# Performance work log

Hardware: AMD Instinct MI355X
Metric: run time of the kernel (lower is better)

Reference implementation:

```python
import jax, jax.numpy as jnp
import numpy as np

LN_EPS = 1e-5
H_STEP = 0.1


def _mm(W, x):
    # conv1d with kernel size 1 == channel matmul: [O,C] x [B,C,N] -> [B,O,N]
    return jnp.einsum('oc,bcn->bon', W, x)


def _layer_norm_all(x):
    # F.layer_norm(x, x.shape): normalize over the ENTIRE tensor, no affine
    m = jnp.mean(x)
    v = jnp.mean((x - m) ** 2)
    return (x - m) * jax.lax.rsqrt(v + LN_EPS)


def double_layer(x, K1, K2):
    # dropout omitted (eval mode / deterministic reference)
    x = _mm(K1, x)
    x = _layer_norm_all(x)
    x = jax.nn.relu(x)
    return _mm(K2, x)


def setup_inputs() -> dict:
    key = jax.random.key(0)
    ks = jax.random.split(key, 16)
    B, XIN, EIN, HID, OUT, NL = 1, 32, 32, 128, 64, 4
    N, E = 50000, 500000
    stdv = 0.001
    inp = {
        'xn': jax.random.normal(ks[0], (B, XIN, N), dtype=jnp.float32),
        'xe': jax.random.normal(ks[1], (B, EIN, E), dtype=jnp.float32),
        'iInd': jax.random.randint(ks[2], (E,), 0, N),
        'jInd': jax.random.randint(ks[3], (E,), 0, N),
        'K1Nopen': jax.random.normal(ks[4], (HID, XIN), dtype=jnp.float32) * stdv,
        'K2Nopen': jax.random.normal(ks[5], (HID, HID), dtype=jnp.float32) * stdv,
        'K1Eopen': jax.random.normal(ks[6], (HID, EIN), dtype=jnp.float32) * stdv,
        'K2Eopen': jax.random.normal(ks[7], (HID, HID), dtype=jnp.float32) * stdv,
        'KNout': jax.random.normal(ks[8], (OUT, HID), dtype=jnp.float32) * stdv,
        'KE1': jax.random.normal(ks[9], (NL, 2 * HID, 3 * HID), dtype=jnp.float32) * stdv,
        'KE2': jax.random.normal(ks[10], (NL, HID, 2 * HID), dtype=jnp.float32) * stdv,
        'KN1': jax.random.normal(ks[11], (NL, 2 * HID, 3 * HID), dtype=jnp.float32) * stdv,
        'KN2': jax.random.normal(ks[12], (NL, HID, 2 * HID), dtype=jnp.float32) * stdv,
    }
    return inp


def reference(xn, xe, iInd, jInd, K1Nopen, K2Nopen, K1Eopen, K2Eopen, KNout,
              KE1, KE2, KN1, KN2):
    xn = double_layer(xn, K1Nopen, K2Nopen)
    xe = double_layer(xe, K1Eopen, K2Eopen)
    N = xn.shape[2]
    # Source sets row = col = Graph.iInd (faithful replication)
    row = iInd
    col = iInd
    nlayers = KE1.shape[0]
    for i in range(nlayers):
        # gather node feats to edges, concat with edge feats: [B, 3*hid, E]
        xec = jnp.concatenate([xn[:, :, row], xn[:, :, col], xe], axis=1)
        xec = double_layer(xec, KE1[i], KE2[i])
        # scatter edge feats back to both endpoints
        zeros = jnp.zeros((xec.shape[0], xec.shape[1], N), dtype=xec.dtype)
        s_i = zeros.at[:, :, iInd].add(xec)
        s_j = zeros.at[:, :, jInd].add(xec)
        ave = 0.5 * (s_i + s_j)          # edgeAve(method='ave')
        div = s_i - s_j                   # edgeDiv
        xnc = jnp.concatenate([ave, div, xn], axis=1)
        xnc = double_layer(xnc, KN1[i], KN2[i])
        xn = xn + H_STEP * xnc
        xe = xe + H_STEP * xec
    xn = _mm(KNout, xn)
    return xn, xe
```

## Files before the change

kernel.cpp:

```cpp
#include <hip/hip_runtime.h>
#include <hip/hip_bf16.h>


typedef __hip_bfloat16 bf16;
typedef __attribute__((ext_vector_type(8))) short bf16x8;
typedef __attribute__((ext_vector_type(4))) float f32x4;

#define HSTEP 0.1f

__device__ __forceinline__ bf16  f2b(float v){ return __float2bfloat16(v); }
__device__ __forceinline__ unsigned int f2bu(float v){
    return (unsigned int)__builtin_bit_cast(unsigned short, __float2bfloat16(v));
}
__device__ __forceinline__ void store8(float* p, const float* a){
    *(float4*)p       = make_float4(a[0],a[1],a[2],a[3]);
    *((float4*)p + 1) = make_float4(a[4],a[5],a[6],a[7]);
}

__device__ __forceinline__ uint4 lnrelu_pack(uint4 r, float mean, float rstd){
    float f0 = __uint_as_float(r.x << 16), f1 = __uint_as_float(r.x & 0xffff0000u);
    float f2 = __uint_as_float(r.y << 16), f3 = __uint_as_float(r.y & 0xffff0000u);
    float f4 = __uint_as_float(r.z << 16), f5 = __uint_as_float(r.z & 0xffff0000u);
    float f6 = __uint_as_float(r.w << 16), f7 = __uint_as_float(r.w & 0xffff0000u);
    f0 = fmaxf(0.f,(f0-mean)*rstd); f1 = fmaxf(0.f,(f1-mean)*rstd);
    f2 = fmaxf(0.f,(f2-mean)*rstd); f3 = fmaxf(0.f,(f3-mean)*rstd);
    f4 = fmaxf(0.f,(f4-mean)*rstd); f5 = fmaxf(0.f,(f5-mean)*rstd);
    f6 = fmaxf(0.f,(f6-mean)*rstd); f7 = fmaxf(0.f,(f7-mean)*rstd);
    uint4 q;
    q.x = f2bu(f0) | (f2bu(f1) << 16);
    q.y = f2bu(f2) | (f2bu(f3) << 16);
    q.z = f2bu(f4) | (f2bu(f5) << 16);
    q.w = f2bu(f6) | (f2bu(f7) << 16);
    return q;
}
__device__ __forceinline__ uint4 pack8f(float4 a, float4 b){
    uint4 q;
    q.x = f2bu(a.x) | (f2bu(a.y) << 16);
    q.y = f2bu(a.z) | (f2bu(a.w) << 16);
    q.z = f2bu(b.x) | (f2bu(b.y) << 16);
    q.w = f2bu(b.z) | (f2bu(b.w) << 16);
    return q;
}

__global__ void wt_transpose(const float* __restrict__ src, float* __restrict__ dst,
                             int O, int C) {
    int i = blockIdx.x*256 + threadIdx.x;
    if (i >= O*C) return;
    int o = i / C, c = i - o*C;
    dst[c*O + o] = src[i];
}

__global__ void wt_ke1_bf(const float* __restrict__ src, bf16* __restrict__ dst) {
    int i = blockIdx.x*256 + threadIdx.x;
    if (i >= 256*256) return;
    int o = i >> 8, c = i & 255;
    float v;
    if (c < 128) v = src[o*384 + c] + src[o*384 + 128 + c];
    else         v = src[o*384 + 128 + c];
    dst[i] = f2b(v);
}

__global__ void wt_cast_bf(const float* __restrict__ src, bf16* __restrict__ dst, int cnt) {
    int i = blockIdx.x*256 + threadIdx.x;
    if (i < cnt) dst[i] = f2b(src[i]);
}

__global__ void csr_hist(const int* __restrict__ ind, int* __restrict__ cnt, int E){
    int e = blockIdx.x*256 + threadIdx.x;
    if (e < E) atomicAdd(&cnt[ind[e]], 1);
}

__global__ void csr_scan(const int* __restrict__ cnt, int* __restrict__ rowptr,
                         int* __restrict__ cursor, int Nn)
{
    __shared__ int part[256];
    int tx = threadIdx.x;
    int chunk = (Nn + 255) / 256;
    int a0 = tx * chunk;
    int a1 = a0 + chunk; if (a1 > Nn) a1 = Nn; if (a0 > Nn) a0 = Nn;
    int s = 0;
    for (int i = a0; i < a1; ++i) s += cnt[i];
    part[tx] = s;
    __syncthreads();
    for (int d = 1; d < 256; d <<= 1) {
        int v = (tx >= d) ? part[tx - d] : 0;
        __syncthreads();
        part[tx] += v;
        __syncthreads();
    }
    int run = (tx == 0) ? 0 : part[tx - 1];
    for (int i = a0; i < a1; ++i) {
        rowptr[i] = run; cursor[i] = run;
        run += cnt[i];
    }
    if (tx == 255) rowptr[Nn] = run;
}

__global__ void csr_fill(const int* __restrict__ ind, int* __restrict__ cursor,
                         int* __restrict__ eadj, int E){
    int e = blockIdx.x*256 + threadIdx.x;
    if (e < E) {
        int p = atomicAdd(&cursor[ind[e]], 1);
        eadj[p] = e;
    }
}

template<bool YB16>
__launch_bounds__(256)
__global__ void gather_nodes(const void* __restrict__ yv,
                             const int* __restrict__ rowptr,
                             const int* __restrict__ eadj,
                             float* __restrict__ s, int Nn)
{
    int wid  = threadIdx.x >> 6;
    int lane = threadIdx.x & 63;
    int node = blockIdx.x * 4 + wid;
    if (node >= Nn) return;
    int k0 = rowptr[node], k1 = rowptr[node+1];
    float a0 = 0.f, a1 = 0.f;
    for (int k = k0; k < k1; ++k) {
        int e = eadj[k];
        if constexpr (YB16) {
            unsigned int b = *((const unsigned int*)yv + (size_t)e*64 + lane);
            a0 += __uint_as_float(b << 16);
            a1 += __uint_as_float(b & 0xffff0000u);
        } else {
            float2 v = *((const float2*)yv + (size_t)e*64 + lane);
            a0 += v.x; a1 += v.y;
        }
    }
    *(float2*)(s + (size_t)node*128 + lane*2) = make_float2(a0, a1);
}

__global__ void ln_reduce(const double* __restrict__ redp, int nb,
                          float* __restrict__ ln, double cnt)
{
    __shared__ double s0[256], s1[256];
    int tx = threadIdx.x;
    double a = 0.0, b = 0.0;
    for (int i = tx; i < nb; i += 256) { a += redp[2*i]; b += redp[2*i+1]; }
    s0[tx] = a; s1[tx] = b;
    __syncthreads();
    for (int s = 128; s > 0; s >>= 1) {
        if (tx < s) { s0[tx] += s0[tx+s]; s1[tx] += s1[tx+s]; }
        __syncthreads();
    }
    if (tx == 0) {
        double m = s0[0] / cnt;
        double var = s1[0] / cnt - m*m;
        if (var < 0.0) var = 0.0;
        ln[0] = (float)m;
        ln[1] = (float)(1.0 / sqrt(var + 1e-5));
    }
}

__launch_bounds__(256)
__global__ void mfma_mm1_edge(const bf16* __restrict__ Wb,
                              const bf16* __restrict__ xnb,
                              const float* __restrict__ xe,
                              const int* __restrict__ iInd,
                              bf16* __restrict__ ucm,
                              int E, double* __restrict__ redp)
{
    __shared__ __align__(16) unsigned short Vs[64*256];
    __shared__ double sred[512];
    const int tx = threadIdx.x;
    const int x0 = blockIdx.x * 64;
    const int e = tx >> 2, q4 = tx & 3;
    const int xedge = x0 + e;
    const bool ev = xedge < E;
    const int gidx = ev ? iInd[xedge] : 0;
    const unsigned swz = (unsigned)((e & 7) << 3);

    #pragma unroll
    for (int p = 0; p < 4; ++p) {
        int k0 = q4*8 + p*32;
        uint4 v = make_uint4(0,0,0,0);
        if (ev) v = *(const uint4*)(xnb + (size_t)gidx*128 + k0);
        *(uint4*)&Vs[(unsigned)(e*256 + k0) ^ swz] = v;
    }
    #pragma unroll
    for (int p = 0; p < 4; ++p) {
        int k0 = q4*8 + p*32;
        uint4 v = make_uint4(0,0,0,0);
        if (ev) {
            const float* s = xe + (size_t)xedge*128 + k0;
            v = pack8f(*(const float4*)s, *(const float4*)(s + 4));
        }
        *(uint4*)&Vs[(unsigned)(e*256 + 128 + k0) ^ swz] = v;
    }
    __syncthreads();

    const int w = tx >> 6, l = tx & 63;
    const int colb = l & 15, grp = l >> 4;
    f32x4 acc[4][4];
    #pragma unroll
    for (int m=0;m<4;++m)
        #pragma unroll
        for (int n=0;n<4;++n) acc[m][n] = (f32x4){0.f,0.f,0.f,0.f};

    #pragma unroll
    for (int kc = 0; kc < 8; ++kc) {
        const int kf = kc*32 + grp*8;
        bf16x8 a[4], b[4];
        #pragma unroll
        for (int m=0;m<4;++m) {
            int row = w*64 + m*16 + colb;
            a[m] = __builtin_bit_cast(bf16x8, *(const uint4*)(Wb + row*256 + kf));
        }
        #pragma unroll
        for (int n=0;n<4;++n) {
            int ee = n*16 + colb;
            b[n] = __builtin_bit_cast(bf16x8,
                     *(const uint4*)&Vs[(unsigned)(ee*256 + kf) ^ (unsigned)((ee&7)<<3)]);
        }
        #pragma unroll
        for (int m=0;m<4;++m)
            #pragma unroll
            for (int n=0;n<4;++n)
                acc[m][n] = __builtin_amdgcn_mfma_f32_16x16x32_bf16(a[m], b[n], acc[m][n], 0, 0, 0);
    }

    double ls = 0.0, ls2 = 0.0;
    const int rq = grp*4;
    #pragma unroll
    for (int n=0;n<4;++n) {
        int edge = x0 + n*16 + colb;
        if (edge < E) {
            #pragma unroll
            for (int m=0;m<4;++m) {
                f32x4 v = acc[m][n];
                int r0 = w*64 + m*16 + rq;
                uint2 q;
                q.x = f2bu(v[0]) | (f2bu(v[1]) << 16);
                q.y = f2bu(v[2]) | (f2bu(v[3]) << 16);
                *(uint2*)(ucm + (size_t)edge*256 + r0) = q;
                ls  += (double)v[0] + (double)v[1] + (double)v[2] + (double)v[3];
                ls2 += (double)v[0]*v[0] + (double)v[1]*v[1]
                     + (double)v[2]*v[2] + (double)v[3]*v[3];
            }
        }
    }
    sred[tx] = ls; sred[256+tx] = ls2;
    __syncthreads();
    for (int s=128; s>0; s>>=1) {
        if (tx < s) { sred[tx] += sred[tx+s]; sred[256+tx] += sred[256+tx+s]; }
        __syncthreads();
    }
    if (tx == 0) {
        redp[2*(size_t)blockIdx.x]     = sred[0];
        redp[2*(size_t)blockIdx.x + 1] = sred[256];
    }
}

__launch_bounds__(256)
__global__ void mfma_mm1_node(const bf16* __restrict__ Wb,
                              const float* __restrict__ si,
                              const float* __restrict__ sj,
                              const float* __restrict__ xn,
                              bf16* __restrict__ ucm,
                              int Nn, double* __restrict__ redp)
{
    __shared__ __align__(16) unsigned short Vs[64*384];
    __shared__ double sred[512];
    const int tx = threadIdx.x;
    const int x0 = blockIdx.x * 64;
    const int e = tx >> 2, q4 = tx & 3;
    const int node = x0 + e;
    const bool nv = node < Nn;
    const unsigned swz = (unsigned)((e & 7) << 3);

    #pragma unroll
    for (int p = 0; p < 4; ++p) {
        int k0 = q4*8 + p*32;
        uint4 va = make_uint4(0,0,0,0), vd = va;
        if (nv) {
            const float* ps = si + (size_t)node*128 + k0;
            const float* pt = sj + (size_t)node*128 + k0;
            float4 a0 = *(const float4*)ps, a1 = *(const float4*)(ps+4);
            float4 b0 = *(const float4*)pt, b1 = *(const float4*)(pt+4);
            float4 av0 = make_float4(0.5f*(a0.x+b0.x),0.5f*(a0.y+b0.y),
                                     0.5f*(a0.z+b0.z),0.5f*(a0.w+b0.w));
            float4 av1 = make_float4(0.5f*(a1.x+b1.x),0.5f*(a1.y+b1.y),
                                     0.5f*(a1.z+b1.z),0.5f*(a1.w+b1.w));
            float4 dv0 = make_float4(a0.x-b0.x,a0.y-b0.y,a0.z-b0.z,a0.w-b0.w);
            float4 dv1 = make_float4(a1.x-b1.x,a1.y-b1.y,a1.z-b1.z,a1.w-b1.w);
            va = pack8f(av0, av1);
            vd = pack8f(dv0, dv1);
        }
        *(uint4*)&Vs[(unsigned)(e*384 + k0) ^ swz] = va;
        *(uint4*)&Vs[(unsigned)(e*384 + 128 + k0) ^ swz] = vd;
    }
    #pragma unroll
    for (int p = 0; p < 4; ++p) {
        int k0 = q4*8 + p*32;
        uint4 v = make_uint4(0,0,0,0);
        if (nv) {
            const float* s = xn + (size_t)node*128 + k0;
            v = pack8f(*(const float4*)s, *(const float4*)(s + 4));
        }
        *(uint4*)&Vs[(unsigned)(e*384 + 256 + k0) ^ swz] = v;
    }
    __syncthreads();

    const int w = tx >> 6, l = tx & 63;
    const int colb = l & 15, grp = l >> 4;
    f32x4 acc[4][4];
    #pragma unroll
    for (int m=0;m<4;++m)
        #pragma unroll
        for (int n=0;n<4;++n) acc[m][n] = (f32x4){0.f,0.f,0.f,0.f};

    #pragma unroll
    for (int kc = 0; kc < 12; ++kc) {
        const int kf = kc*32 + grp*8;
        bf16x8 a[4], b[4];
        #pragma unroll
        for (int m=0;m<4;++m) {
            int row = w*64 + m*16 + colb;
            a[m] = __builtin_bit_cast(bf16x8, *(const uint4*)(Wb + row*384 + kf));
        }
        #pragma unroll
        for (int n=0;n<4;++n) {
            int ee = n*16 + colb;
            b[n] = __builtin_bit_cast(bf16x8,
                     *(const uint4*)&Vs[(unsigned)(ee*384 + kf) ^ (unsigned)((ee&7)<<3)]);
        }
        #pragma unroll
        for (int m=0;m<4;++m)
            #pragma unroll
            for (int n=0;n<4;++n)
                acc[m][n] = __builtin_amdgcn_mfma_f32_16x16x32_bf16(a[m], b[n], acc[m][n], 0, 0, 0);
    }

    double ls = 0.0, ls2 = 0.0;
    const int rq = grp*4;
    #pragma unroll
    for (int n=0;n<4;++n) {
        int nd = x0 + n*16 + colb;
        if (nd < Nn) {
            #pragma unroll
            for (int m=0;m<4;++m) {
                f32x4 v = acc[m][n];
                int r0 = w*64 + m*16 + rq;
                uint2 q;
                q.x = f2bu(v[0]) | (f2bu(v[1]) << 16);
                q.y = f2bu(v[2]) | (f2bu(v[3]) << 16);
                *(uint2*)(ucm + (size_t)nd*256 + r0) = q;
                ls  += (double)v[0] + (double)v[1] + (double)v[2] + (double)v[3];
                ls2 += (double)v[0]*v[0] + (double)v[1]*v[1]
                     + (double)v[2]*v[2] + (double)v[3]*v[3];
            }
        }
    }
    sred[tx] = ls; sred[256+tx] = ls2;
    __syncthreads();
    for (int s=128; s>0; s>>=1) {
        if (tx < s) { sred[tx] += sred[tx+s]; sred[256+tx] += sred[256+tx+s]; }
        __syncthreads();
    }
    if (tx == 0) {
        redp[2*(size_t)blockIdx.x]     = sred[0];
        redp[2*(size_t)blockIdx.x + 1] = sred[256];
    }
}

enum { E2_EDGE = 0, E2_NODE = 1, E2_XE0 = 2, E2_XN0 = 3 };

template<int IC, int EPI, int YM>
__launch_bounds__(256)
__global__ void mfma_mm2(const bf16* __restrict__ Wb2,
                         const bf16* __restrict__ ucm,
                         const float* __restrict__ ln,
                         float* __restrict__ dst,
                         void* __restrict__ yv,
                         bf16* __restrict__ xnb,
                         int n)
{
    __shared__ __align__(16) unsigned short Vs[64*IC];
    const int tx = threadIdx.x;
    const int x0 = blockIdx.x * 64;
    const int e = tx >> 2, q4 = tx & 3;
    const int row = x0 + e;
    const bool rv = row < n;
    const float mean = ln[0], rstd = ln[1];
    const unsigned swz = (unsigned)((e & 7) << 3);

    #pragma unroll
    for (int p = 0; p < IC/32; ++p) {
        int k0 = q4*8 + p*32;
        uint4 v = make_uint4(0,0,0,0);
        if (rv) {
            uint4 r = *(const uint4*)(ucm + (size_t)row*IC + k0);
            v = lnrelu_pack(r, mean, rstd);
        }
        *(uint4*)&Vs[(unsigned)(e*IC + k0) ^ swz] = v;
    }
    __syncthreads();

    const int w = tx >> 6, l = tx & 63;
    const int colb = l & 15, grp = l >> 4;
    f32x4 acc[2][4];
    #pragma unroll
    for (int m=0;m<2;++m)
        #pragma unroll
        for (int nn=0;nn<4;++nn) acc[m][nn] = (f32x4){0.f,0.f,0.f,0.f};

    #pragma unroll
    for (int kc = 0; kc < IC/32; ++kc) {
        const int kf = kc*32 + grp*8;
        bf16x8 a[2], b[4];
        #pragma unroll
        for (int m=0;m<2;++m) {
            int rr = w*32 + m*16 + colb;
            a[m] = __builtin_bit_cast(bf16x8, *(const uint4*)(Wb2 + rr*IC + kf));
        }
        #pragma unroll
        for (int nn=0;nn<4;++nn) {
            int ee = nn*16 + colb;
            b[nn] = __builtin_bit_cast(bf16x8,
                     *(const uint4*)&Vs[(unsigned)(ee*IC + kf) ^ (unsigned)((ee&7)<<3)]);
        }
        #pragma unroll
        for (int m=0;m<2;++m)
            #pragma unroll
            for (int nn=0;nn<4;++nn)
                acc[m][nn] = __builtin_amdgcn_mfma_f32_16x16x32_bf16(a[m], b[nn], acc[m][nn], 0, 0, 0);
    }

    const int rq = grp*4;
    #pragma unroll
    for (int nn=0;nn<4;++nn) {
        int x = x0 + nn*16 + colb;
        if (x < n) {
            #pragma unroll
            for (int m=0;m<2;++m) {
                f32x4 v = acc[m][nn];
                int r0 = w*32 + m*16 + rq;
                if constexpr (EPI == E2_EDGE) {
                    if constexpr (YM == 2) {
                        *(float4*)((float*)yv + (size_t)x*128 + r0) =
                            make_float4(v[0], v[1], v[2], v[3]);
                    } else {
                        uint2 q;
                        q.x = f2bu(v[0]) | (f2bu(v[1]) << 16);
                        q.y = f2bu(v[2]) | (f2bu(v[3]) << 16);
                        *(uint2*)((bf16*)yv + (size_t)x*128 + r0) = q;
                    }
                    float* px = dst + (size_t)x*128 + r0;
                    float4 o = *(float4*)px;
                    o.x += HSTEP*v[0]; o.y += HSTEP*v[1];
                    o.z += HSTEP*v[2]; o.w += HSTEP*v[3];
                    *(float4*)px = o;
                } else if constexpr (EPI == E2_XE0) {
                    *(float4*)(dst + (size_t)x*128 + r0) =
                        make_float4(v[0], v[1], v[2], v[3]);
                } else if constexpr (EPI == E2_NODE) {
                    float* px = dst + (size_t)x*128 + r0;
                    float4 o = *(float4*)px;
                    o.x += HSTEP*v[0]; o.y += HSTEP*v[1];
                    o.z += HSTEP*v[2]; o.w += HSTEP*v[3];
                    *(float4*)px = o;
                    uint2 q;
                    q.x = f2bu(o.x) | (f2bu(o.y) << 16);
                    q.y = f2bu(o.z) | (f2bu(o.w) << 16);
                    *(uint2*)(xnb + (size_t)x*128 + r0) = q;
                } else {
                    *(float4*)(dst + (size_t)x*128 + r0) =
                        make_float4(v[0], v[1], v[2], v[3]);
                    uint2 q;
                    q.x = f2bu(v[0]) | (f2bu(v[1]) << 16);
                    q.y = f2bu(v[2]) | (f2bu(v[3]) << 16);
                    *(uint2*)(xnb + (size_t)x*128 + r0) = q;
                }
            }
        }
    }
}

__launch_bounds__(256)
__global__ void mm1_open(const float* __restrict__ Wt,
                         const float* __restrict__ xin,
                         bf16* __restrict__ ucm,
                         int n, double* __restrict__ redp)
{
    __shared__ float lv[32][64];
    __shared__ double sred[512];
    const int tx = threadIdx.x;
    const int tr = tx & 31, tc = tx >> 5;
    const int x0 = blockIdx.x * 64;

    float acc[4][8];
    #pragma unroll
    for (int ri=0; ri<4; ++ri)
        #pragma unroll
        for (int ei=0; ei<8; ++ei) acc[ri][ei] = 0.f;

    #pragma unroll
    for (int k=0; k<2; ++k) {
        int id = k*256 + tx;
        int xq = id & 15, cc = id >> 4;
        int x = x0 + xq*4;
        const float* p = xin + (size_t)cc*n + x;
        float4 q;
        if (x + 3 < n) q = *(const float4*)p;
        else {
            q.x = (x  <n)?p[0]:0.f; q.y = (x+1<n)?p[1]:0.f;
            q.z = (x+2<n)?p[2]:0.f; q.w = (x+3<n)?p[3]:0.f;
        }
        *(float4*)&lv[cc][xq*4] = q;
    }
    __syncthreads();
    for (int cc=0; cc<32; ++cc) {
        const float* wrow = Wt + cc*128 + tr*4;
        float w[4] = {wrow[0], wrow[1], wrow[2], wrow[3]};
        float vv[8];
        #pragma unroll
        for (int ei=0; ei<8; ++ei) vv[ei] = lv[cc][tc*8+ei];
        #pragma unroll
        for (int ri=0; ri<4; ++ri)
            #pragma unroll
            for (int ei=0; ei<8; ++ei)
                acc[ri][ei] = fmaf(w[ri], vv[ei], acc[ri][ei]);
    }

    double ls = 0.0, ls2 = 0.0;
    #pragma unroll
    for (int ei=0; ei<8; ++ei) {
        int x = x0 + tc*8 + ei;
        if (x < n) {
            uint2 bq;
            bq.x = f2bu(acc[0][ei]) | (f2bu(acc[1][ei]) << 16);
            bq.y = f2bu(acc[2][ei]) | (f2bu(acc[3][ei]) << 16);
            *(uint2*)(ucm + (size_t)x*128 + tr*4) = bq;
            #pragma unroll
            for (int ri=0; ri<4; ++ri) {
                double y = acc[ri][ei]; ls += y; ls2 += y*y;
            }
        }
    }
    sred[tx] = ls; sred[256+tx] = ls2;
    __syncthreads();
    for (int s=128; s>0; s>>=1) {
        if (tx < s) { sred[tx] += sred[tx+s]; sred[256+tx] += sred[256+tx+s]; }
        __syncthreads();
    }
    if (tx == 0) {
        redp[2*(size_t)blockIdx.x]     = sred[0];
        redp[2*(size_t)blockIdx.x + 1] = sred[256];
    }
}

__launch_bounds__(256)
__global__ void final_out(const float* __restrict__ Wt,
                          const float* __restrict__ xncm,
                          float* __restrict__ out, int n)
{
    __shared__ float lv[32][64];
    const int tx = threadIdx.x;
    const int tr = tx & 31, tc = tx >> 5;
    const int x0 = blockIdx.x * 64;

    float acc[2][8];
    #pragma unroll
    for (int ri=0; ri<2; ++ri)
        #pragma unroll
        for (int ei=0; ei<8; ++ei) acc[ri][ei] = 0.f;

    for (int c0 = 0; c0 < 128; c0 += 32) {
        #pragma unroll
        for (int k=0; k<2; ++k) {
            int id = k*256 + tx;
            int xx = id & 63, cg = id >> 6;
            int x = x0 + xx;
            float4 q;
            if (x < n) q = *(const float4*)(xncm + (size_t)x*128 + c0 + cg*4);
            else { q.x=q.y=q.z=q.w=0.f; }
            lv[cg*4+0][xx]=q.x; lv[cg*4+1][xx]=q.y;
            lv[cg*4+2][xx]=q.z; lv[cg*4+3][xx]=q.w;
        }
        __syncthreads();
        for (int cc=0; cc<32; ++cc) {
            const float* wrow = Wt + (c0+cc)*64 + tr*2;
            float w0 = wrow[0], w1 = wrow[1];
            float vv[8];
            #pragma unroll
            for (int ei=0; ei<8; ++ei) vv[ei] = lv[cc][tc*8+ei];
            #pragma unroll
            for (int ei=0; ei<8; ++ei) {
                acc[0][ei] = fmaf(w0, vv[ei], acc[0][ei]);
                acc[1][ei] = fmaf(w1, vv[ei], acc[1][ei]);
            }
        }
        __syncthreads();
    }

    const bool full = (x0 + 64 <= n);
    #pragma unroll
    for (int ri=0; ri<2; ++ri) {
        int r = tr*2 + ri;
        if (full) {
            store8(out + (size_t)r*n + x0 + tc*8, acc[ri]);
        } else {
            #pragma unroll
            for (int ei=0; ei<8; ++ei) {
                int x = x0 + tc*8 + ei;
                if (x < n) out[(size_t)r*n + x] = acc[ri][ei];
            }
        }
    }
}

__launch_bounds__(256)
__global__ void xe_transpose(const float* __restrict__ xe, float* __restrict__ out, int E)
{
    __shared__ float T[128][65];
    const int tx = threadIdx.x;
    const int x0 = blockIdx.x * 64;
    const int es = tx & 63, cg = tx >> 6;
    #pragma unroll
    for (int p = 0; p < 8; ++p) {
        int c = cg*4 + p*16;
        if (x0 + es < E) {
            float4 v = *(const float4*)(xe + (size_t)(x0+es)*128 + c);
            T[c+0][es] = v.x; T[c+1][es] = v.y; T[c+2][es] = v.z; T[c+3][es] = v.w;
        }
    }
    __syncthreads();
    const int c2 = tx >> 1, eo = (tx & 1)*32;
    if (x0 + 64 <= E) {
        #pragma unroll
        for (int q = 0; q < 8; ++q) {
            float4 v = make_float4(T[c2][eo+q*4], T[c2][eo+q*4+1],
                                   T[c2][eo+q*4+2], T[c2][eo+q*4+3]);
            *(float4*)(out + (size_t)c2*E + x0 + eo + q*4) = v;
        }
    } else {
        for (int q = 0; q < 32; ++q) {
            int x = x0 + eo + q;
            if (x < E) out[(size_t)c2*E + x] = T[c2][eo+q];
        }
    }
}

extern "C" void kernel_launch(void* const* d_in, const int* in_sizes, int n_in,
                              void* d_out, int out_size, void* d_ws, size_t ws_size,
                              hipStream_t stream)
{
    const int N = in_sizes[0] / 32;
    const int E = in_sizes[1] / 32;
    const int NL = in_sizes[9] / (256*384);

    const float* xn_in = (const float*)d_in[0];
    const float* xe_in = (const float*)d_in[1];
    const int*   iInd  = (const int*)d_in[2];
    const int*   jInd  = (const int*)d_in[3];
    const float* K1N = (const float*)d_in[4];
    const float* K2N = (const float*)d_in[5];
    const float* K1E = (const float*)d_in[6];
    const float* K2E = (const float*)d_in[7];
    const float* KNo = (const float*)d_in[8];
    const float* KE1 = (const float*)d_in[9];
    const float* KE2 = (const float*)d_in[10];
    const float* KN1 = (const float*)d_in[11];
    const float* KN2 = (const float*)d_in[12];

    char* base = (char*)d_ws;
    size_t off = 0;
    auto carve = [&](size_t bytes)->void* {
        void* p = base + off; off += (bytes + 255) & ~(size_t)255; return p;
    };
    float* xn  = (float*)carve((size_t)128*N*sizeof(float));
    float* xe  = (float*)carve((size_t)128*E*sizeof(float));
    bf16*  u   = (bf16*) carve((size_t)256*E*sizeof(bf16));
    float* si  = (float*)carve((size_t)128*N*sizeof(float));
    float* sj  = (float*)carve((size_t)128*N*sizeof(float));
    float* wtsf= (float*)carve((32*128*2 + 128*64)*sizeof(float));
    bf16*  Wb   = (bf16*)carve((size_t)256*256*sizeof(bf16));
    bf16*  Wb2  = (bf16*)carve((size_t)128*256*sizeof(bf16));
    bf16*  Wn1b = (bf16*)carve((size_t)256*384*sizeof(bf16));
    bf16*  Wn2b = (bf16*)carve((size_t)128*256*sizeof(bf16));
    bf16*  K2Nb = (bf16*)carve((size_t)128*128*sizeof(bf16));
    bf16*  K2Eb = (bf16*)carve((size_t)128*128*sizeof(bf16));
    bf16*  xnb  = (bf16*)carve((size_t)128*N*sizeof(bf16));
    double* redp = (double*)carve(2*8192*sizeof(double));
    float* lnp = (float*)carve(256);
    int* cnt      = (int*)carve((size_t)N*sizeof(int));
    int* rowptr_i = (int*)carve((size_t)(N+1)*sizeof(int));
    int* rowptr_j = (int*)carve((size_t)(N+1)*sizeof(int));
    int* cur_i    = (int*)carve((size_t)N*sizeof(int));
    int* cur_j    = (int*)carve((size_t)N*sizeof(int));
    int* eadj_i   = (int*)carve((size_t)E*sizeof(int));
    int* eadj_j   = (int*)carve((size_t)E*sizeof(int));

    if (ws_size < off) return;

    int ymode = 0;
    void* y = nullptr;
    if (off + (size_t)128*E*sizeof(float) <= ws_size) { y = base + off; ymode = 2; }
    else if (off + (size_t)128*E*sizeof(bf16) <= ws_size) { y = base + off; ymode = 1; }
    if (!ymode) return;

    float* K1Nt = wtsf;
    float* K1Et = K1Nt + 32*128;
    float* KNoT = K1Et + 32*128;

    wt_transpose<<<dim3((128*32 +255)/256),dim3(256),0,stream>>>(K1N, K1Nt, 128, 32);
    wt_transpose<<<dim3((128*32 +255)/256),dim3(256),0,stream>>>(K1E, K1Et, 128, 32);
    wt_transpose<<<dim3((64*128 +255)/256),dim3(256),0,stream>>>(KNo, KNoT, 64, 128);
    wt_cast_bf<<<dim3(64),dim3(256),0,stream>>>(K2N, K2Nb, 128*128);
    wt_cast_bf<<<dim3(64),dim3(256),0,stream>>>(K2E, K2Eb, 128*128);

    const int gN = (N + 63)/64, gE = (E + 63)/64;
    const int gEb = (E + 255)/256;

    (void)hipMemsetAsync(cnt, 0, (size_t)N*sizeof(int), stream);
    csr_hist<<<gEb,256,0,stream>>>(iInd, cnt, E);
    csr_scan<<<1,256,0,stream>>>(cnt, rowptr_i, cur_i, N);
    csr_fill<<<gEb,256,0,stream>>>(iInd, cur_i, eadj_i, E);
    (void)hipMemsetAsync(cnt, 0, (size_t)N*sizeof(int), stream);
    csr_hist<<<gEb,256,0,stream>>>(jInd, cnt, E);
    csr_scan<<<1,256,0,stream>>>(cnt, rowptr_j, cur_j, N);
    csr_fill<<<gEb,256,0,stream>>>(jInd, cur_j, eadj_j, E);

    mm1_open<<<gN,256,0,stream>>>(K1Nt, xn_in, u, N, redp);
    ln_reduce<<<1,256,0,stream>>>(redp, gN, lnp, 128.0*N);
    mfma_mm2<128,E2_XN0,2><<<gN,256,0,stream>>>(K2Nb, u, lnp, xn, nullptr, xnb, N);

    mm1_open<<<gE,256,0,stream>>>(K1Et, xe_in, u, E, redp);
    ln_reduce<<<1,256,0,stream>>>(redp, gE, lnp, 128.0*E);
    mfma_mm2<128,E2_XE0,2><<<gE,256,0,stream>>>(K2Eb, u, lnp, xe, nullptr, nullptr, E);

    for (int l = 0; l < NL; ++l) {
        wt_ke1_bf<<<dim3(256),dim3(256),0,stream>>>(KE1 + (size_t)l*256*384, Wb);
        wt_cast_bf<<<dim3(128),dim3(256),0,stream>>>(KE2 + (size_t)l*128*256, Wb2, 128*256);
        wt_cast_bf<<<dim3(384),dim3(256),0,stream>>>(KN1 + (size_t)l*256*384, Wn1b, 256*384);
        wt_cast_bf<<<dim3(128),dim3(256),0,stream>>>(KN2 + (size_t)l*128*256, Wn2b, 128*256);

        mfma_mm1_edge<<<gE,256,0,stream>>>(Wb, xnb, xe, iInd, u, E, redp);
        ln_reduce<<<1,256,0,stream>>>(redp, gE, lnp, 256.0*E);
        if (ymode == 2) {
            mfma_mm2<256,E2_EDGE,2><<<gE,256,0,stream>>>(Wb2, u, lnp, xe, y, nullptr, E);
            gather_nodes<false><<<(N+3)/4,256,0,stream>>>(y, rowptr_i, eadj_i, si, N);
            gather_nodes<false><<<(N+3)/4,256,0,stream>>>(y, rowptr_j, eadj_j, sj, N);
        } else {
            mfma_mm2<256,E2_EDGE,1><<<gE,256,0,stream>>>(Wb2, u, lnp, xe, y, nullptr, E);
            gather_nodes<true><<<(N+3)/4,256,0,stream>>>(y, rowptr_i, eadj_i, si, N);
            gather_nodes<true><<<(N+3)/4,256,0,stream>>>(y, rowptr_j, eadj_j, sj, N);
        }

        mfma_mm1_node<<<gN,256,0,stream>>>(Wn1b, si, sj, xn, u, N, redp);
        ln_reduce<<<1,256,0,stream>>>(redp, gN, lnp, 256.0*N);
        mfma_mm2<256,E2_NODE,2><<<gN,256,0,stream>>>(Wn2b, u, lnp, xn, nullptr, xnb, N);
    }

    final_out<<<gN,256,0,stream>>>(KNoT, xn, (float*)d_out, N);
    xe_transpose<<<gE,256,0,stream>>>(xe, (float*)d_out + (size_t)64*N, E);
}
```

Before: 4.172 ms.

## Use bf16 edge buffer, unroll gather, stage mm1 stores, prefetch weights, shuffle reductions

The per-edge output y is now always stored as bf16 instead of fp32 when workspace allows, which halves gather traffic and the writes from mm2. The gather loop is unrolled by four with independent accumulators so more loads are in flight. The edge mm1 epilogue stages bf16 results through shared memory to write coalesced 16-byte rows. Weight fragments are double-buffered across k-steps, and the LN block reductions use wave shuffles instead of a shared-memory tree. The bf16 y loses precision relative to the fp32 path.

```diff
diff --git a/kernel.cpp b/kernel.cpp
--- a/kernel.cpp
+++ b/kernel.cpp
@@ -42,6 +42,23 @@
     return q;
 }
 
+__device__ __forceinline__ void block_red2(double ls, double ls2, double* sredw,
+                                           int tx, double* redp, int bid)
+{
+    #pragma unroll
+    for (int off = 32; off; off >>= 1) {
+        ls  += __shfl_down(ls,  off, 64);
+        ls2 += __shfl_down(ls2, off, 64);
+    }
+    const int w = tx >> 6, l = tx & 63;
+    if (l == 0) { sredw[2*w] = ls; sredw[2*w+1] = ls2; }
+    __syncthreads();
+    if (tx == 0) {
+        redp[2*(size_t)bid]     = ((sredw[0]+sredw[2])+(sredw[4]+sredw[6]));
+        redp[2*(size_t)bid + 1] = ((sredw[1]+sredw[3])+(sredw[5]+sredw[7]));
+    }
+}
+
 __global__ void wt_transpose(const float* __restrict__ src, float* __restrict__ dst,
                              int O, int C) {
     int i = blockIdx.x*256 + threadIdx.x;
@@ -105,9 +122,8 @@
     }
 }
 
-template<bool YB16>
 __launch_bounds__(256)
-__global__ void gather_nodes(const void* __restrict__ yv,
+__global__ void gather_nodes(const bf16* __restrict__ y,
                              const int* __restrict__ rowptr,
                              const int* __restrict__ eadj,
                              float* __restrict__ s, int Nn)
@@ -117,18 +133,26 @@
     int node = blockIdx.x * 4 + wid;
     if (node >= Nn) return;
     int k0 = rowptr[node], k1 = rowptr[node+1];
-    float a0 = 0.f, a1 = 0.f;
-    for (int k = k0; k < k1; ++k) {
-        int e = eadj[k];
-        if constexpr (YB16) {
-            unsigned int b = *((const unsigned int*)yv + (size_t)e*64 + lane);
-            a0 += __uint_as_float(b << 16);
-            a1 += __uint_as_float(b & 0xffff0000u);
-        } else {
-            float2 v = *((const float2*)yv + (size_t)e*64 + lane);
-            a0 += v.x; a1 += v.y;
-        }
-    }
+    const unsigned* yu = (const unsigned*)y;
+    float a0=0.f,a1=0.f,b0=0.f,b1=0.f,c0=0.f,c1=0.f,d0=0.f,d1=0.f;
+    int k = k0;
+    for (; k + 4 <= k1; k += 4) {
+        int e0 = eadj[k], e1 = eadj[k+1], e2 = eadj[k+2], e3 = eadj[k+3];
+        unsigned v0 = yu[(size_t)e0*64 + lane];
+        unsigned v1 = yu[(size_t)e1*64 + lane];
+        unsigned v2 = yu[(size_t)e2*64 + lane];
+        unsigned v3 = yu[(size_t)e3*64 + lane];
+        a0 += __uint_as_float(v0 << 16); a1 += __uint_as_float(v0 & 0xffff0000u);
+        b0 += __uint_as_float(v1 << 16); b1 += __uint_as_float(v1 & 0xffff0000u);
+        c0 += __uint_as_float(v2 << 16); c1 += __uint_as_float(v2 & 0xffff0000u);
+        d0 += __uint_as_float(v3 << 16); d1 += __uint_as_float(v3 & 0xffff0000u);
+    }
+    for (; k < k1; ++k) {
+        unsigned v = yu[(size_t)eadj[k]*64 + lane];
+        a0 += __uint_as_float(v << 16); a1 += __uint_as_float(v & 0xffff0000u);
+    }
+    a0 += (b0 + c0) + d0;
+    a1 += (b1 + c1) + d1;
     *(float2*)(s + (size_t)node*128 + lane*2) = make_float2(a0, a1);
 }
 
@@ -163,7 +187,7 @@
                               int E, double* __restrict__ redp)
 {
     __shared__ __align__(16) unsigned short Vs[64*256];
-    __shared__ double sred[512];
+    __shared__ double sredw[8];
     const int tx = threadIdx.x;
     const int x0 = blockIdx.x * 64;
     const int e = tx >> 2, q4 = tx & 3;
@@ -199,15 +223,22 @@
         #pragma unroll
         for (int n=0;n<4;++n) acc[m][n] = (f32x4){0.f,0.f,0.f,0.f};
 
+    const bf16* wp = Wb + (size_t)(w*64 + colb)*256 + grp*8;
+    bf16x8 aC[4], aN[4];
+    #pragma unroll
+    for (int m=0;m<4;++m)
+        aC[m] = __builtin_bit_cast(bf16x8, *(const uint4*)(wp + m*16*256));
+
     #pragma unroll
     for (int kc = 0; kc < 8; ++kc) {
         const int kf = kc*32 + grp*8;
-        bf16x8 a[4], b[4];
-        #pragma unroll
-        for (int m=0;m<4;++m) {
-            int row = w*64 + m*16 + colb;
-            a[m] = __builtin_bit_cast(bf16x8, *(const uint4*)(Wb + row*256 + kf));
-        }
+        if (kc < 7) {
+            #pragma unroll
+            for (int m=0;m<4;++m)
+                aN[m] = __builtin_bit_cast(bf16x8,
+                          *(const uint4*)(wp + m*16*256 + (kc+1)*32));
+        }
+        bf16x8 b[4];
         #pragma unroll
         for (int n=0;n<4;++n) {
             int ee = n*16 + colb;
@@ -218,11 +249,12 @@
         for (int m=0;m<4;++m)
             #pragma unroll
             for (int n=0;n<4;++n)
-                acc[m][n] = __builtin_amdgcn_mfma_f32_16x16x32_bf16(a[m], b[n], acc[m][n], 0, 0, 0);
+                acc[m][n] = __builtin_amdgcn_mfma_f32_16x16x32_bf16(aC[m], b[n], acc[m][n], 0, 0, 0);
+        #pragma unroll
+        for (int m=0;m<4;++m) aC[m] = aN[m];
     }
 
     double ls = 0.0, ls2 = 0.0;
-    const int rq = grp*4;
     #pragma unroll
     for (int n=0;n<4;++n) {
         int edge = x0 + n*16 + colb;
@@ -230,27 +262,38 @@
             #pragma unroll
             for (int m=0;m<4;++m) {
                 f32x4 v = acc[m][n];
-                int r0 = w*64 + m*16 + rq;
-                uint2 q;
-                q.x = f2bu(v[0]) | (f2bu(v[1]) << 16);
-                q.y = f2bu(v[2]) | (f2bu(v[3]) << 16);
-                *(uint2*)(ucm + (size_t)edge*256 + r0) = q;
                 ls  += (double)v[0] + (double)v[1] + (double)v[2] + (double)v[3];
                 ls2 += (double)v[0]*v[0] + (double)v[1]*v[1]
                      + (double)v[2]*v[2] + (double)v[3]*v[3];
             }
         }
     }
-    sred[tx] = ls; sred[256+tx] = ls2;
-    __syncthreads();
-    for (int s=128; s>0; s>>=1) {
-        if (tx < s) { sred[tx] += sred[tx+s]; sred[256+tx] += sred[256+tx+s]; }
-        __syncthreads();
-    }
-    if (tx == 0) {
-        redp[2*(size_t)blockIdx.x]     = sred[0];
-        redp[2*(size_t)blockIdx.x + 1] = sred[256];
-    }
+
+    __syncthreads();
+    const int rq = grp*4;
+    #pragma unroll
+    for (int n=0;n<4;++n) {
+        int ee = n*16 + colb;
+        #pragma unroll
+        for (int m=0;m<4;++m) {
+            f32x4 v = acc[m][n];
+            int r0 = w*64 + m*16 + rq;
+            uint2 q;
+            q.x = f2bu(v[0]) | (f2bu(v[1]) << 16);
+            q.y = f2bu(v[2]) | (f2bu(v[3]) << 16);
+            *(uint2*)&Vs[(unsigned)(ee*256 + r0) ^ (unsigned)((ee&7)<<3)] = q;
+        }
+    }
+    __syncthreads();
+    if (ev) {
+        #pragma unroll
+        for (int p = 0; p < 8; ++p) {
+            int c0 = q4*8 + p*32;
+            uint4 v = *(uint4*)&Vs[(unsigned)(e*256 + c0) ^ swz];
+            *(uint4*)(ucm + (size_t)xedge*256 + c0) = v;
+        }
+    }
+    block_red2(ls, ls2, sredw, tx, redp, blockIdx.x);
 }
 
 __launch_bounds__(256)
@@ -262,7 +305,7 @@
                               int Nn, double* __restrict__ redp)
 {
     __shared__ __align__(16) unsigned short Vs[64*384];
-    __shared__ double sred[512];
+    __shared__ double sredw[8];
     const int tx = threadIdx.x;
     const int x0 = blockIdx.x * 64;
     const int e = tx >> 2, q4 = tx & 3;
@@ -311,15 +354,22 @@
         #pragma unroll
         for (int n=0;n<4;++n) acc[m][n] = (f32x4){0.f,0.f,0.f,0.f};
 
+    const bf16* wp = Wb + (size_t)(w*64 + colb)*384 + grp*8;
+    bf16x8 aC[4], aN[4];
+    #pragma unroll
+    for (int m=0;m<4;++m)
+        aC[m] = __builtin_bit_cast(bf16x8, *(const uint4*)(wp + m*16*384));
+
     #pragma unroll
     for (int kc = 0; kc < 12; ++kc) {
         const int kf = kc*32 + grp*8;
-        bf16x8 a[4], b[4];
-        #pragma unroll
-        for (int m=0;m<4;++m) {
-            int row = w*64 + m*16 + colb;
-            a[m] = __builtin_bit_cast(bf16x8, *(const uint4*)(Wb + row*384 + kf));
-        }
+        if (kc < 11) {
+            #pragma unroll
+            for (int m=0;m<4;++m)
+                aN[m] = __builtin_bit_cast(bf16x8,
+                          *(const uint4*)(wp + m*16*384 + (kc+1)*32));
+        }
+        bf16x8 b[4];
         #pragma unroll
         for (int n=0;n<4;++n) {
             int ee = n*16 + colb;
@@ -330,7 +380,9 @@
         for (int m=0;m<4;++m)
             #pragma unroll
             for (int n=0;n<4;++n)
-                acc[m][n] = __builtin_amdgcn_mfma_f32_16x16x32_bf16(a[m], b[n], acc[m][n], 0, 0, 0);
+                acc[m][n] = __builtin_amdgcn_mfma_f32_16x16x32_bf16(aC[m], b[n], acc[m][n], 0, 0, 0);
+        #pragma unroll
+        for (int m=0;m<4;++m) aC[m] = aN[m];
     }
 
     double ls = 0.0, ls2 = 0.0;
@@ -353,27 +405,18 @@
             }
         }
     }
-    sred[tx] = ls; sred[256+tx] = ls2;
-    __syncthreads();
-    for (int s=128; s>0; s>>=1) {
-        if (tx < s) { sred[tx] += sred[tx+s]; sred[256+tx] += sred[256+tx+s]; }
-        __syncthreads();
-    }
-    if (tx == 0) {
-        redp[2*(size_t)blockIdx.x]     = sred[0];
-        redp[2*(size_t)blockIdx.x + 1] = sred[256];
-    }
+    block_red2(ls, ls2, sredw, tx, redp, blockIdx.x);
 }
 
 enum { E2_EDGE = 0, E2_NODE = 1, E2_XE0 = 2, E2_XN0 = 3 };
 
-template<int IC, int EPI, int YM>
+template<int IC, int EPI>
 __launch_bounds__(256)
 __global__ void mfma_mm2(const bf16* __restrict__ Wb2,
                          const bf16* __restrict__ ucm,
                          const float* __restrict__ ln,
                          float* __restrict__ dst,
-                         void* __restrict__ yv,
+                         bf16* __restrict__ yv,
                          bf16* __restrict__ xnb,
                          int n)
 {
@@ -406,15 +449,22 @@
         #pragma unroll
         for (int nn=0;nn<4;++nn) acc[m][nn] = (f32x4){0.f,0.f,0.f,0.f};
 
+    const bf16* wp = Wb2 + (size_t)(w*32 + colb)*IC + grp*8;
+    bf16x8 aC[2], aN[2];
+    #pragma unroll
+    for (int m=0;m<2;++m)
+        aC[m] = __builtin_bit_cast(bf16x8, *(const uint4*)(wp + m*16*IC));
+
     #pragma unroll
     for (int kc = 0; kc < IC/32; ++kc) {
         const int kf = kc*32 + grp*8;
-        bf16x8 a[2], b[4];
-        #pragma unroll
-        for (int m=0;m<2;++m) {
-            int rr = w*32 + m*16 + colb;
-            a[m] = __builtin_bit_cast(bf16x8, *(const uint4*)(Wb2 + rr*IC + kf));
-        }
+        if (kc < IC/32 - 1) {
+            #pragma unroll
+            for (int m=0;m<2;++m)
+                aN[m] = __builtin_bit_cast(bf16x8,
+                          *(const uint4*)(wp + m*16*IC + (kc+1)*32));
+        }
+        bf16x8 b[4];
         #pragma unroll
         for (int nn=0;nn<4;++nn) {
             int ee = nn*16 + colb;
@@ -425,7 +475,9 @@
         for (int m=0;m<2;++m)
             #pragma unroll
             for (int nn=0;nn<4;++nn)
-                acc[m][nn] = __builtin_amdgcn_mfma_f32_16x16x32_bf16(a[m], b[nn], acc[m][nn], 0, 0, 0);
+                acc[m][nn] = __builtin_amdgcn_mfma_f32_16x16x32_bf16(aC[m], b[nn], acc[m][nn], 0, 0, 0);
+        #pragma unroll
+        for (int m=0;m<2;++m) aC[m] = aN[m];
     }
 
     const int rq = grp*4;
@@ -438,15 +490,10 @@
                 f32x4 v = acc[m][nn];
                 int r0 = w*32 + m*16 + rq;
                 if constexpr (EPI == E2_EDGE) {
-                    if constexpr (YM == 2) {
-                        *(float4*)((float*)yv + (size_t)x*128 + r0) =
-                            make_float4(v[0], v[1], v[2], v[3]);
-                    } else {
-                        uint2 q;
-                        q.x = f2bu(v[0]) | (f2bu(v[1]) << 16);
-                        q.y = f2bu(v[2]) | (f2bu(v[3]) << 16);
-                        *(uint2*)((bf16*)yv + (size_t)x*128 + r0) = q;
-                    }
+                    uint2 q;
+                    q.x = f2bu(v[0]) | (f2bu(v[1]) << 16);
+                    q.y = f2bu(v[2]) | (f2bu(v[3]) << 16);
+                    *(uint2*)(yv + (size_t)x*128 + r0) = q;
                     float* px = dst + (size_t)x*128 + r0;
                     float4 o = *(float4*)px;
                     o.x += HSTEP*v[0]; o.y += HSTEP*v[1];
@@ -485,7 +532,7 @@
                          int n, double* __restrict__ redp)
 {
     __shared__ float lv[32][64];
-    __shared__ double sred[512];
+    __shared__ double sredw[8];
     const int tx = threadIdx.x;
     const int tr = tx & 31, tc = tx >> 5;
     const int x0 = blockIdx.x * 64;
@@ -539,16 +586,7 @@
             }
         }
     }
-    sred[tx] = ls; sred[256+tx] = ls2;
-    __syncthreads();
-    for (int s=128; s>0; s>>=1) {
-        if (tx < s) { sred[tx] += sred[tx+s]; sred[256+tx] += sred[256+tx+s]; }
-        __syncthreads();
-    }
-    if (tx == 0) {
-        redp[2*(size_t)blockIdx.x]     = sred[0];
-        redp[2*(size_t)blockIdx.x + 1] = sred[256];
-    }
+    block_red2(ls, ls2, sredw, tx, redp, blockIdx.x);
 }
 
 __launch_bounds__(256)
@@ -673,6 +711,7 @@
     float* xn  = (float*)carve((size_t)128*N*sizeof(float));
     float* xe  = (float*)carve((size_t)128*E*sizeof(float));
     bf16*  u   = (bf16*) carve((size_t)256*E*sizeof(bf16));
+    bf16*  y   = (bf16*) carve((size_t)128*E*sizeof(bf16));
     float* si  = (float*)carve((size_t)128*N*sizeof(float));
     float* sj  = (float*)carve((size_t)128*N*sizeof(float));
     float* wtsf= (float*)carve((32*128*2 + 128*64)*sizeof(float));
@@ -695,12 +734,6 @@
 
     if (ws_size < off) return;
 
-    int ymode = 0;
-    void* y = nullptr;
-    if (off + (size_t)128*E*sizeof(float) <= ws_size) { y = base + off; ymode = 2; }
-    else if (off + (size_t)128*E*sizeof(bf16) <= ws_size) { y = base + off; ymode = 1; }
-    if (!ymode) return;
-
     float* K1Nt = wtsf;
     float* K1Et = K1Nt + 32*128;
     float* KNoT = K1Et + 32*128;
@@ -725,11 +758,11 @@
 
     mm1_open<<<gN,256,0,stream>>>(K1Nt, xn_in, u, N, redp);
     ln_reduce<<<1,256,0,stream>>>(redp, gN, lnp, 128.0*N);
-    mfma_mm2<128,E2_XN0,2><<<gN,256,0,stream>>>(K2Nb, u, lnp, xn, nullptr, xnb, N);
+    mfma_mm2<128,E2_XN0><<<gN,256,0,stream>>>(K2Nb, u, lnp, xn, nullptr, xnb, N);
 
     mm1_open<<<gE,256,0,stream>>>(K1Et, xe_in, u, E, redp);
     ln_reduce<<<1,256,0,stream>>>(redp, gE, lnp, 128.0*E);
-    mfma_mm2<128,E2_XE0,2><<<gE,256,0,stream>>>(K2Eb, u, lnp, xe, nullptr, nullptr, E);
+    mfma_mm2<128,E2_XE0><<<gE,256,0,stream>>>(K2Eb, u, lnp, xe, nullptr, nullptr, E);
 
     for (int l = 0; l < NL; ++l) {
         wt_ke1_bf<<<dim3(256),dim3(256),0,stream>>>(KE1 + (size_t)l*256*384, Wb);
@@ -739,19 +772,13 @@
 
         mfma_mm1_edge<<<gE,256,0,stream>>>(Wb, xnb, xe, iInd, u, E, redp);
         ln_reduce<<<1,256,0,stream>>>(redp, gE, lnp, 256.0*E);
-        if (ymode == 2) {
-            mfma_mm2<256,E2_EDGE,2><<<gE,256,0,stream>>>(Wb2, u, lnp, xe, y, nullptr, E);
-            gather_nodes<false><<<(N+3)/4,256,0,stream>>>(y, rowptr_i, eadj_i, si, N);
-            gather_nodes<false><<<(N+3)/4,256,0,stream>>>(y, rowptr_j, eadj_j, sj, N);
-        } else {
-            mfma_mm2<256,E2_EDGE,1><<<gE,256,0,stream>>>(Wb2, u, lnp, xe, y, nullptr, E);
-            gather_nodes<true><<<(N+3)/4,256,0,stream>>>(y, rowptr_i, eadj_i, si, N);
-            gather_nodes<true><<<(N+3)/4,256,0,stream>>>(y, rowptr_j, eadj_j, sj, N);
-        }
+        mfma_mm2<256,E2_EDGE><<<gE,256,0,stream>>>(Wb2, u, lnp, xe, y, nullptr, E);
+        gather_nodes<<<(N+3)/4,256,0,stream>>>(y, rowptr_i, eadj_i, si, N);
+        gather_nodes<<<(N+3)/4,256,0,stream>>>(y, rowptr_j, eadj_j, sj, N);
 
         mfma_mm1_node<<<gN,256,0,stream>>>(Wn1b, si, sj, xn, u, N, redp);
         ln_reduce<<<1,256,0,stream>>>(redp, gN, lnp, 256.0*N);
-        mfma_mm2<256,E2_NODE,2><<<gN,256,0,stream>>>(Wn2b, u, lnp, xn, nullptr, xnb, N);
+        mfma_mm2<256,E2_NODE><<<gN,256,0,stream>>>(Wn2b, u, lnp, xn, nullptr, xnb, N);
     }
 
     final_out<<<gN,256,0,stream>>>(KNoT, xn, (float*)d_out, N);
```

New measurement: 3.659 ms. -12.3%, faster.
